# Optimization experiments

Hardware: AMD Instinct MI355X
Metric: run time of the kernel (lower is better)

## Reference

```python
import jax, jax.numpy as jnp
import numpy as np

B, S, D, H = 1024, 64, 1024, 32
HD = D // H  # 32


def make_rpe_map():
    # one-hot map from 225 relative offsets (15x15) to 64x64 (q,k) board pairs
    out = np.zeros((225, 64 * 64), dtype=np.float32)
    for i in range(8):
        for j in range(8):
            for k in range(8):
                for m in range(8):
                    out[15 * (i - k + 7) + (j - m + 7), 64 * (i * 8 + j) + k * 8 + m] = 1
    return out


RPE_MAP = jnp.asarray(make_rpe_map())  # [225, 4096]


def setup_inputs() -> dict:
    key = jax.random.key(0)
    ks = jax.random.split(key, 11)
    s = 0.02
    return {
        "x": jax.random.normal(ks[0], (B, S, D), jnp.float32),
        "q_w": jax.random.normal(ks[1], (D, D), jnp.float32) * s,
        "q_b": jax.random.normal(ks[2], (D,), jnp.float32) * s,
        "k_w": jax.random.normal(ks[3], (D, D), jnp.float32) * s,
        "k_b": jax.random.normal(ks[4], (D,), jnp.float32) * s,
        "v_w": jax.random.normal(ks[5], (D, D), jnp.float32) * s,
        "v_b": jax.random.normal(ks[6], (D,), jnp.float32) * s,
        "out_w": jax.random.normal(ks[7], (D, D), jnp.float32) * s,
        "out_b": jax.random.normal(ks[8], (D,), jnp.float32) * s,
        "rpe_q_w": jax.random.normal(ks[9], (HD * H, 225), jnp.float32) * s,
        "rpe_k_w": jax.random.normal(ks[10], (HD * H, 225), jnp.float32) * s,
    }


def reference(x, q_w, q_b, k_w, k_b, v_w, v_b, out_w, out_b, rpe_q_w, rpe_k_w):
    b, s, _ = x.shape

    def proj(w, bias):
        # torch Linear: y = x @ w.T + b ; then [B,S,H,HD] -> [B,H,S,HD]
        return (x @ w.T + bias).reshape(b, s, H, HD).transpose(0, 2, 1, 3)

    q = proj(q_w, q_b)
    k = proj(k_w, k_b)
    v = proj(v_w, v_b)

    scores = jnp.einsum('bhqd,bhkd->bhqk', q, k)
    bias_q = (rpe_q_w @ RPE_MAP).reshape(HD, H, 64, 64)  # [d,h,q,k]
    scores = scores + jnp.einsum('bhqd,dhqk->bhqk', q, bias_q)
    bias_k = (rpe_k_w @ RPE_MAP).reshape(HD, H, 64, 64)
    scores = scores + jnp.einsum('bhkd,dhqk->bhqk', k, bias_k)
    scores = scores / jnp.sqrt(jnp.asarray(HD, scores.dtype))

    attn = jax.nn.softmax(scores, axis=-1)
    out = jnp.einsum('bhqk,bhkd->bhqd', attn, v)
    out = out.transpose(0, 2, 1, 3).reshape(b, s, D)
    return out @ out_w.T + out_b
```

## Files before the change

### kernel.cpp

```cpp
#include <hip/hip_runtime.h>
#include <hip/hip_bf16.h>

#define AS1 __attribute__((address_space(1)))
#define AS3 __attribute__((address_space(3)))

typedef __attribute__((ext_vector_type(4))) float f32x4;
typedef __attribute__((ext_vector_type(8))) short b16x8;
typedef __attribute__((ext_vector_type(8))) unsigned short u16x8;
typedef unsigned short u16;

static __device__ __forceinline__ u16 f2b(float f) {
  return __builtin_bit_cast(u16, __float2bfloat16(f));
}
static __device__ __forceinline__ float b2f(u16 u) {
  unsigned v = ((unsigned)u) << 16;
  return __builtin_bit_cast(float, v);
}
static __device__ __forceinline__ void gl2lds16(const u16* g, u16* l) {
  __builtin_amdgcn_global_load_lds((const AS1 void*)g, (AS3 void*)l, 16, 0, 0);
}

__global__ void k_cvt(const float* __restrict__ s, u16* __restrict__ d, long n) {
  long i = ((long)blockIdx.x * 256 + threadIdx.x) * 8;
  if (i >= n) return;
  float4 a = *(const float4*)(s + i);
  float4 b = *(const float4*)(s + i + 4);
  u16x8 o;
  o[0] = f2b(a.x); o[1] = f2b(a.y); o[2] = f2b(a.z); o[3] = f2b(a.w);
  o[4] = f2b(b.x); o[5] = f2b(b.y); o[6] = f2b(b.z); o[7] = f2b(b.w);
  *(u16x8*)(d + i) = o;
}

__global__ void k_rpe(const float* __restrict__ rq, const float* __restrict__ rk,
                      u16* __restrict__ oq, u16* __restrict__ ok) {
  int h = blockIdx.y;
  int r = blockIdx.x * 8 + (threadIdx.x >> 5);
  int d = threadIdx.x & 31;
  const float* s = blockIdx.z ? rk : rq;
  u16* o = blockIdx.z ? ok : oq;
  float v = (r < 225) ? s[(d * 32 + h) * 225 + r] : 0.f;
  o[(h * 240 + r) * 32 + d] = f2b(v);
}

template <int MODE>
__global__ __launch_bounds__(512) void k_gemm(
    const u16* __restrict__ A, const u16* __restrict__ Bw,
    const float* __restrict__ b0, const float* __restrict__ b1, const float* __restrict__ b2,
    u16* __restrict__ oq, float* __restrict__ of) {
  __shared__ alignas(16) u16 lds[4][16384];
  const int tid = threadIdx.x;
  const int l = tid & 63, w = tid >> 6;
  const int lo = l & 15, hi = l >> 4;
  const int wr = w >> 2, wc = w & 3;

  const int nbx = gridDim.x;
  const int nb = nbx * gridDim.y;
  const int bid = blockIdx.y * nbx + blockIdx.x;
  const int ord = (bid & 7) * (nb >> 3) + (bid >> 3);
  const int tn = (ord % nbx) * 256, tm = (ord / nbx) * 256;

  const int sl = (tid & 7) ^ ((tid >> 3) & 7);
  const int srow = 2 * (tid >> 3) + (sl >> 2);
  const int scol = (sl & 3) * 8;
  const u16* gA = A + (size_t)(tm + srow) * 1024 + scol;
  const u16* gB = Bw + (size_t)(tn + srow) * 1024 + scol;
  u16* dst = &lds[0][0] + tid * 8;

  const int p7 = (lo >> 1) & 7;
  const int slr = ((lo & 1) * 4 + hi) ^ p7;
  const int aoff = wr * 4096 + (lo >> 1) * 64 + slr * 8;
  const int boff = 8192 + wc * 2048 + (lo >> 1) * 64 + slr * 8;

  f32x4 acc[8][4];
#pragma unroll
  for (int i = 0; i < 8; ++i)
#pragma unroll
    for (int j = 0; j < 4; ++j) acc[i][j] = (f32x4){0.f, 0.f, 0.f, 0.f};

  b16x8 af[8], bf[4];

#define STG_A(t) { const int kc = (t) * 32; u16* d = dst + ((t) & 3) * 16384; \
    gl2lds16(gA + kc, d);  gl2lds16(gA + 131072 + kc, d + 4096); }
#define STG_B(t) { const int kc = (t) * 32; u16* d = dst + ((t) & 3) * 16384; \
    gl2lds16(gB + kc, d + 8192);  gl2lds16(gB + 131072 + kc, d + 12288); }
#define PHA(bi) { const u16* _b = &lds[0][0] + (bi) * 16384; \
    _Pragma("unroll") for (int _i = 0; _i < 4; ++_i) af[_i] = *(const b16x8*)(_b + aoff + _i * 512); \
    _Pragma("unroll") for (int _j = 0; _j < 4; ++_j) bf[_j] = *(const b16x8*)(_b + boff + _j * 512); \
    __builtin_amdgcn_s_barrier(); \
    asm volatile("s_waitcnt lgkmcnt(0)" ::: "memory"); \
    __builtin_amdgcn_sched_barrier(0); \
    __builtin_amdgcn_s_setprio(1); \
    _Pragma("unroll") for (int _i = 0; _i < 4; ++_i) \
    _Pragma("unroll") for (int _j = 0; _j < 4; ++_j) \
      acc[_i][_j] = __builtin_amdgcn_mfma_f32_16x16x32_bf16(af[_i], bf[_j], acc[_i][_j], 0, 0, 0); \
    __builtin_amdgcn_s_setprio(0); \
    __builtin_amdgcn_s_barrier(); }
#define PHB(bi) { const u16* _b = &lds[0][0] + (bi) * 16384; \
    _Pragma("unroll") for (int _i = 4; _i < 8; ++_i) af[_i] = *(const b16x8*)(_b + aoff + _i * 512); \
    __builtin_amdgcn_s_barrier(); \
    asm volatile("s_waitcnt lgkmcnt(0)" ::: "memory"); \
    __builtin_amdgcn_sched_barrier(0); \
    __builtin_amdgcn_s_setprio(1); \
    _Pragma("unroll") for (int _i = 4; _i < 8; ++_i) \
    _Pragma("unroll") for (int _j = 0; _j < 4; ++_j) \
      acc[_i][_j] = __builtin_amdgcn_mfma_f32_16x16x32_bf16(af[_i], bf[_j], acc[_i][_j], 0, 0, 0); \
    __builtin_amdgcn_s_setprio(0); }
#define WV(n) { asm volatile("s_waitcnt vmcnt(" #n ")" ::: "memory"); \
    __builtin_amdgcn_s_barrier(); asm volatile("" ::: "memory"); }

  STG_A(0) STG_B(0) STG_A(1) STG_B(1) STG_A(2) STG_B(2)
  asm volatile("s_waitcnt vmcnt(8)" ::: "memory");
  __builtin_amdgcn_s_barrier();
  asm volatile("" ::: "memory");

#pragma unroll 4
  for (int kt = 0; kt < 28; ++kt) {
    STG_A(kt + 3)
    PHA(kt & 3)
    STG_B(kt + 3)
    PHB(kt & 3)
    WV(8)
  }
  STG_A(31) PHA(0) STG_B(31) PHB(0) WV(8)
  PHA(1) PHB(1) WV(4)
  PHA(2) PHB(2) WV(0)
  PHA(3) PHB(3)
#undef STG_A
#undef STG_B
#undef PHA
#undef PHB
#undef WV

  if (MODE == 0) {
    const size_t G = 67108864;
    const int g = tn >> 10;
    const float* bias = (g == 0) ? b0 : (g == 1) ? b1 : b2;
    const int nn0 = (tn & 1023) + wc * 64;
#pragma unroll
    for (int j = 0; j < 4; ++j) {
      const int nn = nn0 + j * 16 + lo;
      const float bv = bias[nn];
      const int h = nn >> 5, hd = nn & 31;
      if (g < 2) {
#pragma unroll
        for (int i = 0; i < 8; ++i) {
          const int m0 = tm + wr * 128 + i * 16 + hi * 4;
          const int b = m0 >> 6, s0 = m0 & 63;
          const size_t base = (size_t)g * G + ((size_t)(b * 32 + h) * 64 + s0) * 32 + hd;
#pragma unroll
          for (int r = 0; r < 4; ++r) oq[base + (size_t)r * 32] = f2b(acc[i][j][r] + bv);
        }
      } else {
#pragma unroll
        for (int i = 0; i < 8; ++i) {
          const int m0 = tm + wr * 128 + i * 16 + hi * 4;
          const int b = m0 >> 6, s0 = m0 & 63;
          ushort4 pk;
          pk.x = f2b(acc[i][j][0] + bv);
          pk.y = f2b(acc[i][j][1] + bv);
          pk.z = f2b(acc[i][j][2] + bv);
          pk.w = f2b(acc[i][j][3] + bv);
          *(ushort4*)(oq + 2 * G + ((size_t)(b * 32 + h) * 32 + hd) * 64 + s0) = pk;
        }
      }
    }
  } else {
#pragma unroll
    for (int j = 0; j < 4; ++j) {
      const int n = tn + wc * 64 + j * 16 + lo;
      const float bv = b0[n];
#pragma unroll
      for (int i = 0; i < 8; ++i) {
        const int m0 = tm + wr * 128 + i * 16 + hi * 4;
#pragma unroll
        for (int r = 0; r < 4; ++r) of[(size_t)(m0 + r) * 1024 + n] = acc[i][j][r] + bv;
      }
    }
  }
}

__global__ __launch_bounds__(256) void k_attn(
    const u16* __restrict__ qkv, const u16* __restrict__ rq,
    const u16* __restrict__ rk, u16* __restrict__ att) {
  __shared__ alignas(16) u16 board[16 * 240 * 4];
  u16* pl = board;
  const int l = threadIdx.x & 63, w = threadIdx.x >> 6;
  const int lo = l & 15, hi = l >> 4;
  const int b = blockIdx.x, h = blockIdx.y;
  const size_t G = 67108864;
  const u16* qp = qkv + (size_t)(b * 32 + h) * 2048;
  const u16* kp = qkv + G + (size_t)(b * 32 + h) * 2048;
  const u16* vp = qkv + 2 * G + (size_t)(b * 32 + h) * 2048;

  b16x8 qf = *(const b16x8*)(qp + (w * 16 + lo) * 32 + hi * 8);
  b16x8 v00 = *(const b16x8*)(vp + lo * 64 + hi * 8);
  b16x8 v01 = *(const b16x8*)(vp + lo * 64 + 32 + hi * 8);
  b16x8 v10 = *(const b16x8*)(vp + (16 + lo) * 64 + hi * 8);
  b16x8 v11 = *(const b16x8*)(vp + (16 + lo) * 64 + 32 + hi * 8);

  f32x4 s0[4];
#pragma unroll
  for (int kt = 0; kt < 4; ++kt) {
    b16x8 kf = *(const b16x8*)(kp + (kt * 16 + lo) * 32 + hi * 8);
    f32x4 z = (f32x4){0.f, 0.f, 0.f, 0.f};
    s0[kt] = __builtin_amdgcn_mfma_f32_16x16x32_bf16(qf, kf, z, 0, 0, 0);
  }

  const u16* rqh = rq + (size_t)h * 7680;
#pragma unroll
  for (int nt = 0; nt < 15; ++nt) {
    b16x8 rf = *(const b16x8*)(rqh + (nt * 16 + lo) * 32 + hi * 8);
    f32x4 z = (f32x4){0.f, 0.f, 0.f, 0.f};
    f32x4 c = __builtin_amdgcn_mfma_f32_16x16x32_bf16(qf, rf, z, 0, 0, 0);
    ushort4 pk;
    pk.x = f2b(c[0]); pk.y = f2b(c[1]); pk.z = f2b(c[2]); pk.w = f2b(c[3]);
    *(ushort4*)(board + (((w * 4 + hi) * 240 + nt * 16 + lo) << 2)) = pk;
  }
#pragma unroll
  for (int kt = 0; kt < 4; ++kt)
#pragma unroll
    for (int r = 0; r < 4; ++r) {
      int q = w * 16 + hi * 4 + r, k = kt * 16 + lo;
      int rel = 15 * ((q >> 3) - (k >> 3) + 7) + (q & 7) - (k & 7) + 7;
      s0[kt][r] += b2f(board[((w * 4 + hi) * 240 + rel) * 4 + r]);
    }

  b16x8 kfa = *(const b16x8*)(kp + (w * 16 + lo) * 32 + hi * 8);
  const u16* rkh = rk + (size_t)h * 7680;
#pragma unroll
  for (int nt = 0; nt < 15; ++nt) {
    b16x8 rf = *(const b16x8*)(rkh + (nt * 16 + lo) * 32 + hi * 8);
    f32x4 z = (f32x4){0.f, 0.f, 0.f, 0.f};
    f32x4 c = __builtin_amdgcn_mfma_f32_16x16x32_bf16(kfa, rf, z, 0, 0, 0);
    ushort4 pk;
    pk.x = f2b(c[0]); pk.y = f2b(c[1]); pk.z = f2b(c[2]); pk.w = f2b(c[3]);
    *(ushort4*)(board + (((w * 4 + hi) * 240 + nt * 16 + lo) << 2)) = pk;
  }
  __syncthreads();
#pragma unroll
  for (int kt = 0; kt < 4; ++kt)
#pragma unroll
    for (int r = 0; r < 4; ++r) {
      int q = w * 16 + hi * 4 + r, k = kt * 16 + lo;
      int rel = 15 * ((q >> 3) - (k >> 3) + 7) + (q & 7) - (k & 7) + 7;
      s0[kt][r] += b2f(board[((k >> 2) * 240 + rel) * 4 + (k & 3)]);
    }

  const float sc = 0.17677669529663689f;
#pragma unroll
  for (int kt = 0; kt < 4; ++kt) s0[kt] *= sc;
  float p[4][4], rsum[4];
#pragma unroll
  for (int r = 0; r < 4; ++r) {
    float m = s0[0][r];
    m = fmaxf(m, s0[1][r]); m = fmaxf(m, s0[2][r]); m = fmaxf(m, s0[3][r]);
    m = fmaxf(m, __shfl_xor(m, 1));
    m = fmaxf(m, __shfl_xor(m, 2));
    m = fmaxf(m, __shfl_xor(m, 4));
    m = fmaxf(m, __shfl_xor(m, 8));
    float sum = 0.f;
#pragma unroll
    for (int kt = 0; kt < 4; ++kt) {
      float e = __expf(s0[kt][r] - m);
      p[kt][r] = e;
      sum += e;
    }
    sum += __shfl_xor(sum, 1);
    sum += __shfl_xor(sum, 2);
    sum += __shfl_xor(sum, 4);
    sum += __shfl_xor(sum, 8);
    rsum[r] = 1.f / sum;
  }

  __syncthreads();

#pragma unroll
  for (int kt = 0; kt < 4; ++kt)
#pragma unroll
    for (int r = 0; r < 4; ++r) pl[(w * 16 + hi * 4 + r) * 72 + kt * 16 + lo] = f2b(p[kt][r]);

  f32x4 o0 = (f32x4){0.f, 0.f, 0.f, 0.f}, o1 = (f32x4){0.f, 0.f, 0.f, 0.f};
  {
    b16x8 pa0 = *(const b16x8*)(pl + (w * 16 + lo) * 72 + hi * 8);
    b16x8 pa1 = *(const b16x8*)(pl + (w * 16 + lo) * 72 + 32 + hi * 8);
    o0 = __builtin_amdgcn_mfma_f32_16x16x32_bf16(pa0, v00, o0, 0, 0, 0);
    o1 = __builtin_amdgcn_mfma_f32_16x16x32_bf16(pa0, v10, o1, 0, 0, 0);
    o0 = __builtin_amdgcn_mfma_f32_16x16x32_bf16(pa1, v01, o0, 0, 0, 0);
    o1 = __builtin_amdgcn_mfma_f32_16x16x32_bf16(pa1, v11, o1, 0, 0, 0);
  }

#pragma unroll
  for (int r = 0; r < 4; ++r) {
    int q = w * 16 + hi * 4 + r;
    size_t base = (size_t)(b * 64 + q) * 1024 + h * 32;
    att[base + lo] = f2b(o0[r] * rsum[r]);
    att[base + 16 + lo] = f2b(o1[r] * rsum[r]);
  }
}

extern "C" void kernel_launch(void* const* d_in, const int* in_sizes, int n_in,
                              void* d_out, int out_size, void* d_ws, size_t ws_size,
                              hipStream_t stream) {
  const float* x   = (const float*)d_in[0];
  const float* qw  = (const float*)d_in[1];
  const float* qb  = (const float*)d_in[2];
  const float* kw  = (const float*)d_in[3];
  const float* kb  = (const float*)d_in[4];
  const float* vw  = (const float*)d_in[5];
  const float* vb  = (const float*)d_in[6];
  const float* ow  = (const float*)d_in[7];
  const float* ob  = (const float*)d_in[8];
  const float* rqw = (const float*)d_in[9];
  const float* rkw = (const float*)d_in[10];

  if (ws_size < 680460288ULL) return;
  char* p = (char*)d_ws;
  u16* ws_x   = (u16*)p; p += (size_t)65536 * 1024 * 2;
  u16* ws_w   = (u16*)p; p += (size_t)3 * 1024 * 1024 * 2;
  u16* ws_wo  = (u16*)p; p += (size_t)1024 * 1024 * 2;
  u16* ws_rq  = (u16*)p; p += (size_t)32 * 240 * 32 * 2;
  u16* ws_rk  = (u16*)p; p += (size_t)32 * 240 * 32 * 2;
  u16* ws_qkv = (u16*)p; p += (size_t)3 * 67108864 * 2;
  u16* ws_att = (u16*)p; p += (size_t)65536 * 1024 * 2;

  k_cvt<<<32768, 256, 0, stream>>>(x, ws_x, 67108864L);
  k_cvt<<<512, 256, 0, stream>>>(qw, ws_w, 1048576L);
  k_cvt<<<512, 256, 0, stream>>>(kw, ws_w + 1048576, 1048576L);
  k_cvt<<<512, 256, 0, stream>>>(vw, ws_w + 2097152, 1048576L);
  k_cvt<<<512, 256, 0, stream>>>(ow, ws_wo, 1048576L);
  k_rpe<<<dim3(30, 32, 2), 256, 0, stream>>>(rqw, rkw, ws_rq, ws_rk);

  k_gemm<0><<<dim3(12, 256), 512, 0, stream>>>(ws_x, ws_w, qb, kb, vb, ws_qkv, nullptr);
  k_attn<<<dim3(1024, 32), 256, 0, stream>>>(ws_qkv, ws_rq, ws_rk, ws_att);
  k_gemm<1><<<dim3(4, 256), 512, 0, stream>>>(ws_att, ws_wo, ob, nullptr, nullptr, nullptr,
                                              (float*)d_out);
}
```

Before: 1.009 ms.

## Shrink GEMM M-tile to 128 and load B fragments directly from global

The GEMM block tile drops from 256x256 to 128x256 and only the A operand is staged through LDS. Each wave now loads its B fragments straight from global memory into registers instead of through LDS. This cuts LDS use from 128KB to 32KB, requests 4 blocks per CU via launch bounds, and doubles the grid, aiming for higher occupancy and fewer LDS round trips. The cost is less operand reuse per block, more global/L2 traffic for B, and global-load latency exposed inside the loop.

```diff
diff --git a/kernel.cpp b/kernel.cpp
--- a/kernel.cpp
+++ b/kernel.cpp
@@ -43,11 +43,11 @@
 }
 
 template <int MODE>
-__global__ __launch_bounds__(512) void k_gemm(
+__global__ __launch_bounds__(512, 4) void k_gemm(
     const u16* __restrict__ A, const u16* __restrict__ Bw,
     const float* __restrict__ b0, const float* __restrict__ b1, const float* __restrict__ b2,
     u16* __restrict__ oq, float* __restrict__ of) {
-  __shared__ alignas(16) u16 lds[4][16384];
+  __shared__ alignas(16) u16 lds[4][4096];
   const int tid = threadIdx.x;
   const int l = tid & 63, w = tid >> 6;
   const int lo = l & 15, hi = l >> 4;
@@ -57,79 +57,62 @@
   const int nb = nbx * gridDim.y;
   const int bid = blockIdx.y * nbx + blockIdx.x;
   const int ord = (bid & 7) * (nb >> 3) + (bid >> 3);
-  const int tn = (ord % nbx) * 256, tm = (ord / nbx) * 256;
+  const int tn = (ord % nbx) * 256, tm = (ord / nbx) * 128;
 
   const int sl = (tid & 7) ^ ((tid >> 3) & 7);
   const int srow = 2 * (tid >> 3) + (sl >> 2);
   const int scol = (sl & 3) * 8;
   const u16* gA = A + (size_t)(tm + srow) * 1024 + scol;
-  const u16* gB = Bw + (size_t)(tn + srow) * 1024 + scol;
-  u16* dst = &lds[0][0] + tid * 8;
 
   const int p7 = (lo >> 1) & 7;
   const int slr = ((lo & 1) * 4 + hi) ^ p7;
-  const int aoff = wr * 4096 + (lo >> 1) * 64 + slr * 8;
-  const int boff = 8192 + wc * 2048 + (lo >> 1) * 64 + slr * 8;
-
-  f32x4 acc[8][4];
-#pragma unroll
-  for (int i = 0; i < 8; ++i)
+  const int aoff = wr * 2048 + (lo >> 1) * 64 + slr * 8;
+
+  const u16* bp = Bw + (size_t)(tn + wc * 64 + lo) * 1024 + hi * 8;
+
+  f32x4 acc[4][4];
+#pragma unroll
+  for (int i = 0; i < 4; ++i)
 #pragma unroll
     for (int j = 0; j < 4; ++j) acc[i][j] = (f32x4){0.f, 0.f, 0.f, 0.f};
 
-  b16x8 af[8], bf[4];
-
-#define STG_A(t) { const int kc = (t) * 32; u16* d = dst + ((t) & 3) * 16384; \
-    gl2lds16(gA + kc, d);  gl2lds16(gA + 131072 + kc, d + 4096); }
-#define STG_B(t) { const int kc = (t) * 32; u16* d = dst + ((t) & 3) * 16384; \
-    gl2lds16(gB + kc, d + 8192);  gl2lds16(gB + 131072 + kc, d + 12288); }
-#define PHA(bi) { const u16* _b = &lds[0][0] + (bi) * 16384; \
-    _Pragma("unroll") for (int _i = 0; _i < 4; ++_i) af[_i] = *(const b16x8*)(_b + aoff + _i * 512); \
-    _Pragma("unroll") for (int _j = 0; _j < 4; ++_j) bf[_j] = *(const b16x8*)(_b + boff + _j * 512); \
-    __builtin_amdgcn_s_barrier(); \
+#define STG_A(t) gl2lds16(gA + (t) * 32, &lds[(t) & 3][0] + tid * 8);
+#define BODY(t, STG_STMT, VMC) { \
+    b16x8 bc[4]; \
+    _Pragma("unroll") for (int _j = 0; _j < 4; ++_j) \
+      bc[_j] = *(const b16x8*)(bp + _j * 16384 + (t) * 32); \
+    __builtin_amdgcn_sched_barrier(0); \
+    STG_STMT \
+    const u16* _ab = &lds[(t) & 3][0]; \
+    b16x8 fa[4]; \
+    _Pragma("unroll") for (int _i = 0; _i < 4; ++_i) \
+      fa[_i] = *(const b16x8*)(_ab + aoff + _i * 512); \
+    asm volatile("s_waitcnt vmcnt(" #VMC ")" ::: "memory"); \
     asm volatile("s_waitcnt lgkmcnt(0)" ::: "memory"); \
     __builtin_amdgcn_sched_barrier(0); \
     __builtin_amdgcn_s_setprio(1); \
     _Pragma("unroll") for (int _i = 0; _i < 4; ++_i) \
     _Pragma("unroll") for (int _j = 0; _j < 4; ++_j) \
-      acc[_i][_j] = __builtin_amdgcn_mfma_f32_16x16x32_bf16(af[_i], bf[_j], acc[_i][_j], 0, 0, 0); \
-    __builtin_amdgcn_s_setprio(0); \
-    __builtin_amdgcn_s_barrier(); }
-#define PHB(bi) { const u16* _b = &lds[0][0] + (bi) * 16384; \
-    _Pragma("unroll") for (int _i = 4; _i < 8; ++_i) af[_i] = *(const b16x8*)(_b + aoff + _i * 512); \
-    __builtin_amdgcn_s_barrier(); \
-    asm volatile("s_waitcnt lgkmcnt(0)" ::: "memory"); \
-    __builtin_amdgcn_sched_barrier(0); \
-    __builtin_amdgcn_s_setprio(1); \
-    _Pragma("unroll") for (int _i = 4; _i < 8; ++_i) \
-    _Pragma("unroll") for (int _j = 0; _j < 4; ++_j) \
-      acc[_i][_j] = __builtin_amdgcn_mfma_f32_16x16x32_bf16(af[_i], bf[_j], acc[_i][_j], 0, 0, 0); \
+      acc[_i][_j] = __builtin_amdgcn_mfma_f32_16x16x32_bf16(fa[_i], bc[_j], acc[_i][_j], 0, 0, 0); \
     __builtin_amdgcn_s_setprio(0); }
-#define WV(n) { asm volatile("s_waitcnt vmcnt(" #n ")" ::: "memory"); \
-    __builtin_amdgcn_s_barrier(); asm volatile("" ::: "memory"); }
-
-  STG_A(0) STG_B(0) STG_A(1) STG_B(1) STG_A(2) STG_B(2)
-  asm volatile("s_waitcnt vmcnt(8)" ::: "memory");
+#define EB { __builtin_amdgcn_s_barrier(); asm volatile("" ::: "memory"); }
+
+  STG_A(0) STG_A(1) STG_A(2)
+  asm volatile("s_waitcnt vmcnt(1)" ::: "memory");
   __builtin_amdgcn_s_barrier();
   asm volatile("" ::: "memory");
 
-#pragma unroll 4
   for (int kt = 0; kt < 28; ++kt) {
-    STG_A(kt + 3)
-    PHA(kt & 3)
-    STG_B(kt + 3)
-    PHB(kt & 3)
-    WV(8)
-  }
-  STG_A(31) PHA(0) STG_B(31) PHB(0) WV(8)
-  PHA(1) PHB(1) WV(4)
-  PHA(2) PHB(2) WV(0)
-  PHA(3) PHB(3)
+    BODY(kt, STG_A(kt + 3), 1)
+    EB
+  }
+  BODY(28, STG_A(31), 1) EB
+  BODY(29, , 0) EB
+  BODY(30, , 0) EB
+  BODY(31, , 0)
 #undef STG_A
-#undef STG_B
-#undef PHA
-#undef PHB
-#undef WV
+#undef BODY
+#undef EB
 
   if (MODE == 0) {
     const size_t G = 67108864;
@@ -143,8 +126,8 @@
       const int h = nn >> 5, hd = nn & 31;
       if (g < 2) {
 #pragma unroll
-        for (int i = 0; i < 8; ++i) {
-          const int m0 = tm + wr * 128 + i * 16 + hi * 4;
+        for (int i = 0; i < 4; ++i) {
+          const int m0 = tm + wr * 64 + i * 16 + hi * 4;
           const int b = m0 >> 6, s0 = m0 & 63;
           const size_t base = (size_t)g * G + ((size_t)(b * 32 + h) * 64 + s0) * 32 + hd;
 #pragma unroll
@@ -152,8 +135,8 @@
         }
       } else {
 #pragma unroll
-        for (int i = 0; i < 8; ++i) {
-          const int m0 = tm + wr * 128 + i * 16 + hi * 4;
+        for (int i = 0; i < 4; ++i) {
+          const int m0 = tm + wr * 64 + i * 16 + hi * 4;
           const int b = m0 >> 6, s0 = m0 & 63;
           ushort4 pk;
           pk.x = f2b(acc[i][j][0] + bv);
@@ -170,8 +153,8 @@
       const int n = tn + wc * 64 + j * 16 + lo;
       const float bv = b0[n];
 #pragma unroll
-      for (int i = 0; i < 8; ++i) {
-        const int m0 = tm + wr * 128 + i * 16 + hi * 4;
+      for (int i = 0; i < 4; ++i) {
+        const int m0 = tm + wr * 64 + i * 16 + hi * 4;
 #pragma unroll
         for (int r = 0; r < 4; ++r) of[(size_t)(m0 + r) * 1024 + n] = acc[i][j][r] + bv;
       }
@@ -330,8 +313,8 @@
   k_cvt<<<512, 256, 0, stream>>>(ow, ws_wo, 1048576L);
   k_rpe<<<dim3(30, 32, 2), 256, 0, stream>>>(rqw, rkw, ws_rq, ws_rk);
 
-  k_gemm<0><<<dim3(12, 256), 512, 0, stream>>>(ws_x, ws_w, qb, kb, vb, ws_qkv, nullptr);
+  k_gemm<0><<<dim3(12, 512), 512, 0, stream>>>(ws_x, ws_w, qb, kb, vb, ws_qkv, nullptr);
   k_attn<<<dim3(1024, 32), 256, 0, stream>>>(ws_qkv, ws_rq, ws_rk, ws_att);
-  k_gemm<1><<<dim3(4, 256), 512, 0, stream>>>(ws_att, ws_wo, ob, nullptr, nullptr, nullptr,
+  k_gemm<1><<<dim3(4, 512), 512, 0, stream>>>(ws_att, ws_wo, ob, nullptr, nullptr, nullptr,
                                               (float*)d_out);
 }
```

Result: slower. 1.623 ms (+60.9%).
